# Kernel tuning notes

Measured on AMD Instinct MI355X. Metric: run time of the kernel, lower is better.

Reference implementation:

```python
import jax, jax.numpy as jnp
import numpy as np


def setup_inputs() -> dict:
    key = jax.random.key(0)
    k1, k2, k3 = jax.random.split(key, 3)
    B, C, L, R = 64, 256, 4096, 16
    x = jax.random.normal(k1, (B, C, L), dtype=jnp.float32)
    # Linear weights with kaiming-ish scale
    w1 = jax.random.normal(k2, (R, C), dtype=jnp.float32) * (1.0 / np.sqrt(C))
    b1 = jnp.zeros((R,), dtype=jnp.float32)
    w2 = jax.random.normal(k3, (C, R), dtype=jnp.float32) * (1.0 / np.sqrt(R))
    b2 = jnp.zeros((C,), dtype=jnp.float32)
    return {"x": x, "w1": w1, "b1": b1, "w2": w2, "b2": b2}


def reference(x, w1, b1, w2, b2):
    # squeeze: global average pool over length -> [B, C]
    y = jnp.mean(x, axis=2)
    # excitation: 2-layer MLP gate
    y = jax.nn.relu(jnp.einsum('bc,rc->br', y, w1) + b1)      # [B, C/r]
    y = jax.nn.sigmoid(jnp.einsum('br,cr->bc', y, w2) + b2)   # [B, C]
    # scale: channel-wise broadcast multiply
    return x * y[:, :, None]
```

## Files before the change

### kernel.cpp

```cpp
#include <hip/hip_runtime.h>
#include <math.h>

#define SE_B 64
#define SE_C 256
#define SE_L 4096
#define SE_R 16

typedef float vf4 __attribute__((ext_vector_type(4)));

__global__ __launch_bounds__(256) void se_mean_kernel(
    const float* __restrict__ x, float* __restrict__ means) {
  const int row = blockIdx.x;
  const int t = threadIdx.x;
  const vf4* __restrict__ xrow =
      reinterpret_cast<const vf4*>(x + (size_t)row * SE_L);
  float s = 0.0f;
#pragma unroll
  for (int i = 0; i < 4; ++i) {
    vf4 v = xrow[t + i * 256];
    s += (v.x + v.y) + (v.z + v.w);
  }
#pragma unroll
  for (int off = 32; off > 0; off >>= 1) s += __shfl_down(s, off, 64);
  __shared__ float partial[4];
  if ((t & 63) == 0) partial[t >> 6] = s;
  __syncthreads();
  if (t == 0) {
    float tot = (partial[0] + partial[1]) + (partial[2] + partial[3]);
    means[row] = tot * (1.0f / SE_L);
  }
}

__global__ __launch_bounds__(256) void se_gate_kernel(
    const float* __restrict__ means, const float* __restrict__ w1,
    const float* __restrict__ b1, const float* __restrict__ w2,
    const float* __restrict__ b2, float* __restrict__ gates) {
  const int b = blockIdx.x;
  const int t = threadIdx.x;
  __shared__ float m[SE_C];
  __shared__ float y[SE_R];
  m[t] = means[b * SE_C + t];
  __syncthreads();
  if (t < SE_R) {
    float acc = b1[t];
    const float* __restrict__ w1r = w1 + t * SE_C;
#pragma unroll 8
    for (int c = 0; c < SE_C; ++c) acc += m[c] * w1r[c];
    y[t] = fmaxf(acc, 0.0f);
  }
  __syncthreads();
  float g = b2[t];
  const float* __restrict__ w2r = w2 + t * SE_R;
#pragma unroll
  for (int r = 0; r < SE_R; ++r) g += y[r] * w2r[r];
  gates[b * SE_C + t] = 1.0f / (1.0f + expf(-g));
}

__global__ __launch_bounds__(256) void se_scale_kernel(
    const float* __restrict__ x, const float* __restrict__ gates,
    float* __restrict__ out) {
  const size_t n4 = (size_t)SE_B * SE_C * (SE_L / 4);
  const size_t stride = (size_t)gridDim.x * blockDim.x;
  const vf4* __restrict__ x4 = reinterpret_cast<const vf4*>(x);
  vf4* __restrict__ o4 = reinterpret_cast<vf4*>(out);
  for (size_t i = (size_t)blockIdx.x * blockDim.x + threadIdx.x; i < n4;
       i += stride) {
    const int row = (int)(i >> 10);
    const float g = gates[row];
    vf4 v = x4[i];
    v *= g;
    __builtin_nontemporal_store(v, &o4[i]);
  }
}

extern "C" void kernel_launch(void* const* d_in, const int* in_sizes, int n_in,
                              void* d_out, int out_size, void* d_ws,
                              size_t ws_size, hipStream_t stream) {
  const float* x = (const float*)d_in[0];
  const float* w1 = (const float*)d_in[1];
  const float* b1 = (const float*)d_in[2];
  const float* w2 = (const float*)d_in[3];
  const float* b2 = (const float*)d_in[4];
  float* out = (float*)d_out;

  float* means = (float*)d_ws;
  float* gates = means + SE_B * SE_C;

  se_mean_kernel<<<SE_B * SE_C, 256, 0, stream>>>(x, means);
  se_gate_kernel<<<SE_B, SE_C, 0, stream>>>(means, w1, b1, w2, b2, gates);
  se_scale_kernel<<<2048, 256, 0, stream>>>(x, gates, out);
}
```

Baseline: 131.6 us.

## Fuse gate into scale and pipeline mean/scale over batch chunks

```diff
diff --git a/kernel.cpp b/kernel.cpp
--- a/kernel.cpp
+++ b/kernel.cpp
@@ -6,70 +6,89 @@
 #define SE_L 4096
 #define SE_R 16
 
+#define CHUNK_B 8
+#define NCHUNK (SE_B / CHUNK_B)
+#define CHUNK_ROWS (CHUNK_B * SE_C)
+
 typedef float vf4 __attribute__((ext_vector_type(4)));
 
-__global__ __launch_bounds__(256) void se_mean_kernel(
-    const float* __restrict__ x, float* __restrict__ means) {
-  const int row = blockIdx.x;
+__global__ __launch_bounds__(256) void se_fused(
+    const float* __restrict__ x, const float* __restrict__ w1,
+    const float* __restrict__ b1, const float* __restrict__ w2,
+    const float* __restrict__ b2, float* __restrict__ out,
+    float* __restrict__ means, int mean_base, int scale_base, int both) {
   const int t = threadIdx.x;
-  const vf4* __restrict__ xrow =
-      reinterpret_cast<const vf4*>(x + (size_t)row * SE_L);
-  float s = 0.0f;
+  int role, idx;
+  if (both) {
+    role = blockIdx.x & 1;
+    idx = blockIdx.x >> 1;
+  } else {
+    role = (mean_base >= 0) ? 0 : 1;
+    idx = blockIdx.x;
+  }
+
+  __shared__ float m_lds[SE_C];
+  __shared__ float yp[SE_R][SE_R + 1];
+  __shared__ float y_lds[SE_R];
+  __shared__ float red[4];
+
+  if (role == 0) {
+    const int row = mean_base + idx;
+    const vf4* __restrict__ xrow =
+        reinterpret_cast<const vf4*>(x + (size_t)row * SE_L);
+    float s = 0.0f;
 #pragma unroll
-  for (int i = 0; i < 4; ++i) {
-    vf4 v = xrow[t + i * 256];
-    s += (v.x + v.y) + (v.z + v.w);
-  }
+    for (int i = 0; i < 4; ++i) {
+      vf4 v = xrow[t + (i << 8)];
+      s += (v.x + v.y) + (v.z + v.w);
+    }
 #pragma unroll
-  for (int off = 32; off > 0; off >>= 1) s += __shfl_down(s, off, 64);
-  __shared__ float partial[4];
-  if ((t & 63) == 0) partial[t >> 6] = s;
-  __syncthreads();
-  if (t == 0) {
-    float tot = (partial[0] + partial[1]) + (partial[2] + partial[3]);
-    means[row] = tot * (1.0f / SE_L);
-  }
-}
+    for (int off = 32; off > 0; off >>= 1) s += __shfl_down(s, off, 64);
+    if ((t & 63) == 0) red[t >> 6] = s;
+    __syncthreads();
+    if (t == 0) {
+      float tot = (red[0] + red[1]) + (red[2] + red[3]);
+      means[row] = tot * (1.0f / SE_L);
+    }
+  } else {
+    const int row = scale_base + idx;
+    const int c = row & (SE_C - 1);
 
-__global__ __launch_bounds__(256) void se_gate_kernel(
-    const float* __restrict__ means, const float* __restrict__ w1,
-    const float* __restrict__ b1, const float* __restrict__ w2,
-    const float* __restrict__ b2, float* __restrict__ gates) {
-  const int b = blockIdx.x;
-  const int t = threadIdx.x;
-  __shared__ float m[SE_C];
-  __shared__ float y[SE_R];
-  m[t] = means[b * SE_C + t];
-  __syncthreads();
-  if (t < SE_R) {
-    float acc = b1[t];
-    const float* __restrict__ w1r = w1 + t * SE_C;
-#pragma unroll 8
-    for (int c = 0; c < SE_C; ++c) acc += m[c] * w1r[c];
-    y[t] = fmaxf(acc, 0.0f);
-  }
-  __syncthreads();
-  float g = b2[t];
-  const float* __restrict__ w2r = w2 + t * SE_R;
+    m_lds[t] = means[row - c + t];
+    __syncthreads();
+
+    const int g = t >> 4, j = t & 15;
+    float part = 0.0f;
+    const float* __restrict__ w1g = w1 + (g << 8);
 #pragma unroll
-  for (int r = 0; r < SE_R; ++r) g += y[r] * w2r[r];
-  gates[b * SE_C + t] = 1.0f / (1.0f + expf(-g));
-}
+    for (int k = 0; k < 16; ++k) {
+      const int ch = j + (k << 4);
+      part += m_lds[ch] * w1g[ch];
+    }
+    yp[g][j] = part;
+    __syncthreads();
+    if (t < SE_R) {
+      float acc = b1[t];
+#pragma unroll
+      for (int k = 0; k < 16; ++k) acc += yp[t][k];
+      y_lds[t] = fmaxf(acc, 0.0f);
+    }
+    __syncthreads();
 
-__global__ __launch_bounds__(256) void se_scale_kernel(
-    const float* __restrict__ x, const float* __restrict__ gates,
-    float* __restrict__ out) {
-  const size_t n4 = (size_t)SE_B * SE_C * (SE_L / 4);
-  const size_t stride = (size_t)gridDim.x * blockDim.x;
-  const vf4* __restrict__ x4 = reinterpret_cast<const vf4*>(x);
-  vf4* __restrict__ o4 = reinterpret_cast<vf4*>(out);
-  for (size_t i = (size_t)blockIdx.x * blockDim.x + threadIdx.x; i < n4;
-       i += stride) {
-    const int row = (int)(i >> 10);
-    const float g = gates[row];
-    vf4 v = x4[i];
-    v *= g;
-    __builtin_nontemporal_store(v, &o4[i]);
+    float gg = b2[c];
+    const float* __restrict__ w2c = w2 + (c << 4);
+#pragma unroll
+    for (int r = 0; r < SE_R; ++r) gg += y_lds[r] * w2c[r];
+    gg = 1.0f / (1.0f + expf(-gg));
+
+    const vf4* __restrict__ xrow =
+        reinterpret_cast<const vf4*>(x + (size_t)row * SE_L);
+    vf4* __restrict__ orow = reinterpret_cast<vf4*>(out + (size_t)row * SE_L);
+#pragma unroll
+    for (int i = 0; i < 4; ++i) {
+      vf4 v = xrow[t + (i << 8)];
+      __builtin_nontemporal_store(v * gg, &orow[t + (i << 8)]);
+    }
   }
 }
 
@@ -82,11 +101,18 @@
   const float* w2 = (const float*)d_in[3];
   const float* b2 = (const float*)d_in[4];
   float* out = (float*)d_out;
+  float* means = (float*)d_ws;
 
-  float* means = (float*)d_ws;
-  float* gates = means + SE_B * SE_C;
-
-  se_mean_kernel<<<SE_B * SE_C, 256, 0, stream>>>(x, means);
-  se_gate_kernel<<<SE_B, SE_C, 0, stream>>>(means, w1, b1, w2, b2, gates);
-  se_scale_kernel<<<2048, 256, 0, stream>>>(x, gates, out);
+  se_fused<<<CHUNK_ROWS, 256, 0, stream>>>(x, w1, b1, w2, b2, out, means,
+                                           0, -1,
+                                           0);
+  for (int k = 1; k < NCHUNK; ++k) {
+    se_fused<<<2 * CHUNK_ROWS, 256, 0, stream>>>(
+        x, w1, b1, w2, b2, out, means,
+        k * CHUNK_ROWS, (k - 1) * CHUNK_ROWS,
+        1);
+  }
+  se_fused<<<CHUNK_ROWS, 256, 0, stream>>>(
+      x, w1, b1, w2, b2, out, means,
+      -1, (NCHUNK - 1) * CHUNK_ROWS, 0);
 }
```

Result: slower. 153.4 us (+16.6%).
